# Kernel tuning notes

Measured on AMD Instinct MI355X. Metric: run time of the kernel, lower is better.

The kernel has to match this reference:

```python
import jax, jax.numpy as jnp
import numpy as np

N, E, H, EF, DIM = 50000, 800000, 128, 16, 3
MF = 2 * H + EF + 1 + DIM  # dist_l2 (1) + dist_abs (DIM) = 276


def setup_inputs() -> dict:
    key = jax.random.key(0)
    ks = jax.random.split(key, 16)
    w = lambda k, shape, s=0.05: (jax.random.normal(k, shape, jnp.float32) * s)
    return dict(
        h=jax.random.normal(ks[0], (N, H), jnp.float32),
        coords=jax.random.normal(ks[1], (N, DIM), jnp.float32),
        a=jax.random.normal(ks[2], (E, EF), jnp.float32),
        src=jax.random.randint(ks[3], (E,), 0, N),
        dst=jax.random.randint(ks[4], (E,), 0, N),
        We1=w(ks[5], (MF, H)), be1=jnp.zeros((H,), jnp.float32),
        We2=w(ks[6], (H, H)), be2=jnp.zeros((H,), jnp.float32),
        Wa=w(ks[7], (H, 1)), ba=jnp.zeros((1,), jnp.float32),
        Wn1=w(ks[8], (2 * H, H)), bn1=jnp.zeros((H,), jnp.float32),
        Wn2=w(ks[9], (H, H)), bn2=jnp.zeros((H,), jnp.float32),
        Wc1=w(ks[10], (MF, H)), bc1=jnp.zeros((H,), jnp.float32),
        Wc2=w(ks[11], (H, H)), bc2=jnp.zeros((H,), jnp.float32),
        Wc3=w(ks[12], (H, 1), 0.001),  # xavier gain=0.001, no bias
    )


def reference(h, coords, a, src, dst,
              We1, be1, We2, be2, Wa, ba,
              Wn1, bn1, Wn2, bn2,
              Wc1, bc1, Wc2, bc2, Wc3):
    act = jax.nn.silu
    # gather node data onto edges
    xs, xd = coords[src], coords[dst]          # [E, DIM]
    diffs = xs - xd                            # [E, DIM]
    radials = jnp.linalg.norm(diffs, axis=-1, keepdims=True)  # dist_l2
    D = jnp.concatenate([radials, jnp.abs(diffs)], axis=-1)   # dist_l2, dist_abs
    f = jnp.concatenate([h[src], h[dst], D, a], axis=-1)      # [E, MF]
    # coord_mlp: Lin-act-Lin-act-Lin(no bias)
    cm = act(f @ Wc1 + bc1)
    cm = act(cm @ Wc2 + bc2)
    cm = cm @ Wc3                              # [E, 1]
    msg_x = cm * diffs / (radials + 1.0)       # [E, DIM]
    # edge_mlp + attention gate
    mh = act(f @ We1 + be1)
    mh = act(mh @ We2 + be2)                   # [E, H]
    att = jax.nn.sigmoid(mh @ Wa + ba)         # [E, 1]
    msg_h = att * mh
    # scatter-sum to destination nodes
    x_agg = jax.ops.segment_sum(msg_x, dst, num_segments=N)
    h_agg = jax.ops.segment_sum(msg_h, dst, num_segments=N)
    coords_out = coords + x_agg
    nh = act(jnp.concatenate([h, h_agg], axis=-1) @ Wn1 + bn1) @ Wn2 + bn2
    h_out = h + nh
    return h_out, coords_out
```

## Files before the change

kernel.cpp:

```cpp
#include <hip/hip_runtime.h>
#include <math.h>

#define HH 128
#define HP 64

typedef __attribute__((ext_vector_type(8))) short short8;
typedef __attribute__((ext_vector_type(4))) float float4v;
typedef __attribute__((ext_vector_type(4))) unsigned uint4v;

__device__ __forceinline__ float blo(unsigned w){ return __uint_as_float(w << 16); }
__device__ __forceinline__ float bhi(unsigned w){ return __uint_as_float(w & 0xffff0000u); }
__device__ __forceinline__ unsigned short f2b(float x){
  unsigned u = __float_as_uint(x);
  u += 0x7fffu + ((u >> 16) & 1u);
  return (unsigned short)(u >> 16);
}
__device__ __forceinline__ unsigned pack2(float a, float b){
  return (unsigned)f2b(a) | ((unsigned)f2b(b) << 16);
}
__device__ __forceinline__ float silu_f(float x){ return x / (1.f + __expf(-x)); }

__global__ __launch_bounds__(256, 2) void precompute_mfma_kernel(
    const float* __restrict__ h,
    const float* __restrict__ We1, const float* __restrict__ be1,
    const float* __restrict__ Wc1, const float* __restrict__ bc1,
    unsigned* __restrict__ A1, unsigned* __restrict__ B1,
    unsigned* __restrict__ Ac, unsigned* __restrict__ Bc, int N)
{
  __shared__ unsigned short hs[2][16 * 136];

  const int t = threadIdx.x;
  const int lane = t & 63;
  const int w = t >> 6;
  const int col = lane & 15;
  const int quad = lane >> 4;

  const float* Wsel = (w < 2) ? We1 : Wc1;
  const int kb = (w & 1) * 128;
  unsigned* outp = (w == 0) ? A1 : (w == 1) ? B1 : (w == 2) ? Ac : Bc;
  const float* biasp = (w == 0) ? be1 : (w == 2) ? bc1 : nullptr;

  uint4v wf[8][4];
  #pragma unroll
  for (int nt = 0; nt < 8; ++nt) {
    const int cn = nt * 16 + col;
    #pragma unroll
    for (int ks = 0; ks < 4; ++ks) {
      unsigned u[4];
      #pragma unroll
      for (int i = 0; i < 4; ++i) {
        const int k0 = kb + ks * 32 + quad * 8 + 2 * i;
        u[i] = pack2(Wsel[(size_t)k0 * 128 + cn], Wsel[(size_t)(k0 + 1) * 128 + cn]);
      }
      wf[nt][ks] = (uint4v){u[0], u[1], u[2], u[3]};
    }
  }
  float bias[8];
  #pragma unroll
  for (int nt = 0; nt < 8; ++nt) bias[nt] = biasp ? biasp[nt * 16 + col] : 0.f;

  const int ntiles = (N + 15) >> 4;
  auto stage = [&](int tl, int b) {
    const int n0s = tl * 16;
    for (int idx = t; idx < 16 * 64; idx += 256) {
      const int row = idx >> 6, jp = idx & 63;
      const int n = min(n0s + row, N - 1);
      float2 hv = ((const float2*)h)[(size_t)n * 64 + jp];
      ((unsigned*)&hs[b][row * 136])[jp] = pack2(hv.x, hv.y);
    }
  };

  int tile = blockIdx.x;
  if (tile < ntiles) stage(tile, 0);
  int buf = 0;
  for (; tile < ntiles; tile += gridDim.x, buf ^= 1) {
    __syncthreads();
    if (tile + (int)gridDim.x < ntiles) stage(tile + gridDim.x, buf ^ 1);

    float4v acc[8] = {{0,0,0,0},{0,0,0,0},{0,0,0,0},{0,0,0,0},
                      {0,0,0,0},{0,0,0,0},{0,0,0,0},{0,0,0,0}};
    #pragma unroll
    for (int ks = 0; ks < 4; ++ks) {
      short8 af = __builtin_bit_cast(short8,
          *(const uint4v*)&hs[buf][col * 136 + ks * 32 + quad * 8]);
      #pragma unroll
      for (int nt = 0; nt < 8; ++nt)
        acc[nt] = __builtin_amdgcn_mfma_f32_16x16x32_bf16(
            af, __builtin_bit_cast(short8, wf[nt][ks]), acc[nt], 0, 0, 0);
    }
    const int n0 = tile * 16;
    #pragma unroll
    for (int nt = 0; nt < 8; ++nt) {
      #pragma unroll
      for (int r = 0; r < 4; ++r) {
        float v = acc[nt][r] + bias[nt];
        float o = __shfl_xor(v, 1, 64);
        const int node = n0 + quad * 4 + r;
        if (!(lane & 1) && node < N)
          outp[(size_t)node * HP + ((nt * 16 + col) >> 1)] = pack2(v, o);
      }
    }
  }
}

template<int MODE>
__global__ __launch_bounds__(256, 3) void edge_kernel(
    const unsigned* __restrict__ Apart, const unsigned* __restrict__ Bpart,
    const float* __restrict__ W1,
    const float* __restrict__ W2, const float* __restrict__ b2,
    const float* __restrict__ Wv,
    const float* __restrict__ ba_p,
    const int* __restrict__ src, const int* __restrict__ dst,
    const float* __restrict__ coords, const float* __restrict__ afeat,
    float* __restrict__ out_agg, int E)
{
  __shared__ unsigned short W2Ts[128 * 136];
  __shared__ unsigned short mhl16[32 * 136];
  __shared__ unsigned short tailsA[32 * 40];
  __shared__ float    dif[32 * 4];
  __shared__ int      sl[32], dl[32];
  __shared__ float    p_lds[4][16];

  const int t = threadIdx.x;
  const int lane = t & 63;
  const int w = t >> 6;
  const int mtile = w >> 1;
  const int nhalf = w & 1;
  const int col = lane & 15;
  const int quad = lane >> 4;

  for (int i = t; i < 128 * 128; i += 256) {
    int k = i >> 7, n = i & 127;
    W2Ts[n * 136 + k] = f2b(W2[i]);
  }
  for (int i = t; i < 32 * 20; i += 256) ((unsigned*)tailsA)[i] = 0u;

  uint4v wtf[4];
  #pragma unroll
  for (int nt = 0; nt < 4; ++nt) {
    const int n = nhalf * 64 + nt * 16 + col;
    unsigned u[4];
    #pragma unroll
    for (int i = 0; i < 4; ++i) {
      const int k0 = quad * 8 + 2 * i;
      float a = (k0     < 20) ? W1[(size_t)(256 + k0    ) * 128 + n] : 0.f;
      float b = (k0 + 1 < 20) ? W1[(size_t)(256 + k0 + 1) * 128 + n] : 0.f;
      u[i] = pack2(a, b);
    }
    wtf[nt] = (uint4v){u[0], u[1], u[2], u[3]};
  }
  float b2reg[4], wvreg[4];
  #pragma unroll
  for (int nt = 0; nt < 4; ++nt) {
    const int n = (nhalf * 4 + nt) * 16 + col;
    b2reg[nt] = b2[n];
    wvreg[nt] = Wv[n];
  }
  const float bav = (MODE == 0) ? ba_p[0] : 0.f;
  __syncthreads();

  const int ntiles = (E + 31) >> 5;
  for (int tile = blockIdx.x; tile < ntiles; tile += gridDim.x) {
    const int e0 = tile * 32;
    if (t < 32) {
      int eg = e0 + t;
      int s = 0, d = 0;
      if (eg < E) { s = src[eg]; d = dst[eg]; }
      sl[t] = s; dl[t] = d;
      float dx = coords[s*3+0] - coords[d*3+0];
      float dy = coords[s*3+1] - coords[d*3+1];
      float dz = coords[s*3+2] - coords[d*3+2];
      float rad = sqrtf(dx*dx + dy*dy + dz*dz);
      dif[t*4+0] = dx; dif[t*4+1] = dy; dif[t*4+2] = dz; dif[t*4+3] = rad;
      unsigned* ta = (unsigned*)&tailsA[t * 40];
      ta[0] = pack2(rad, fabsf(dx));
      ta[1] = pack2(fabsf(dy), fabsf(dz));
    }
    #pragma unroll
    for (int i = t; i < 512; i += 256) {
      int e = i >> 4, f = i & 15;
      int eg = e0 + e;
      tailsA[e * 40 + 4 + f] =
          (eg < E) ? f2b(afeat[(size_t)eg * 16 + f]) : (unsigned short)0;
    }
    __syncthreads();

    int er[4], sidx[4], didx[4];
    #pragma unroll
    for (int r = 0; r < 4; ++r) {
      er[r] = mtile * 16 + quad * 4 + r;
      sidx[r] = sl[er[r]]; didx[r] = dl[er[r]];
    }
    const int jbase = nhalf * 32 + (col >> 1);
    unsigned wa32[4][4], wb32[4][4];
    #pragma unroll
    for (int r = 0; r < 4; ++r) {
      const unsigned* ap = Apart + (size_t)sidx[r] * HP + jbase;
      const unsigned* bp = Bpart + (size_t)didx[r] * HP + jbase;
      #pragma unroll
      for (int nt = 0; nt < 4; ++nt) { wa32[r][nt] = ap[nt * 8]; wb32[r][nt] = bp[nt * 8]; }
    }

    float4v acct[4] = {{0,0,0,0},{0,0,0,0},{0,0,0,0},{0,0,0,0}};
    {
      const unsigned short* ap = &tailsA[(mtile * 16 + col) * 40 + quad * 8];
      short8 af = __builtin_bit_cast(short8, *(const uint4v*)ap);
      #pragma unroll
      for (int nt = 0; nt < 4; ++nt)
        acct[nt] = __builtin_amdgcn_mfma_f32_16x16x32_bf16(
            af, __builtin_bit_cast(short8, wtf[nt]), acct[nt], 0, 0, 0);
    }

    const bool hiSel = (col & 1);
    #pragma unroll
    for (int r = 0; r < 4; ++r) {
      #pragma unroll
      for (int nt = 0; nt < 4; ++nt) {
        float va = hiSel ? bhi(wa32[r][nt]) : blo(wa32[r][nt]);
        float vb = hiSel ? bhi(wb32[r][nt]) : blo(wb32[r][nt]);
        float v = va + vb + acct[nt][r];
        mhl16[er[r] * 136 + nhalf * 64 + nt * 16 + col] = f2b(silu_f(v));
      }
    }
    __syncthreads();

    float4v acc[4] = {{0,0,0,0},{0,0,0,0},{0,0,0,0},{0,0,0,0}};
    {
      const unsigned short* abase = &mhl16[(mtile * 16 + col) * 136 + quad * 8];
      #pragma unroll
      for (int ks = 0; ks < 4; ++ks) {
        short8 af = __builtin_bit_cast(short8, *(const uint4v*)(abase + ks * 32));
        #pragma unroll
        for (int nt = 0; nt < 4; ++nt) {
          const unsigned short* bp =
              &W2Ts[((nhalf * 4 + nt) * 16 + col) * 136 + ks * 32 + quad * 8];
          short8 bf = __builtin_bit_cast(short8, *(const uint4v*)bp);
          acc[nt] = __builtin_amdgcn_mfma_f32_16x16x32_bf16(af, bf, acc[nt], 0, 0, 0);
        }
      }
    }

    float p[4] = {0.f, 0.f, 0.f, 0.f};
    #pragma unroll
    for (int nt = 0; nt < 4; ++nt)
      #pragma unroll
      for (int r = 0; r < 4; ++r) {
        float v = silu_f(acc[nt][r] + b2reg[nt]);
        acc[nt][r] = v;
        p[r] += v * wvreg[nt];
      }
    #pragma unroll
    for (int r = 0; r < 4; ++r) {
      #pragma unroll
      for (int off = 1; off < 16; off <<= 1) p[r] += __shfl_xor(p[r], off, 64);
    }
    if (col == 0) {
      #pragma unroll
      for (int r = 0; r < 4; ++r) p_lds[w][quad * 4 + r] = p[r];
    }
    __syncthreads();

    #pragma unroll
    for (int r = 0; r < 4; ++r) {
      const int le = quad * 4 + r;
      const int ei = mtile * 16 + le;
      const int eg = e0 + ei;
      const float pfull = p_lds[w][le] + p_lds[w ^ 1][le];
      if (MODE == 0) {
        if (eg < E) {
          float att = 1.f / (1.f + __expf(-(pfull + bav)));
          int d = dl[ei];
          #pragma unroll
          for (int nt = 0; nt < 4; ++nt) {
            int n = (nhalf * 4 + nt) * 16 + col;
            unsafeAtomicAdd(&out_agg[(size_t)d * HH + n], att * acc[nt][r]);
          }
        }
      } else {
        if (nhalf == 0 && eg < E && col < 3) {
          float rad = dif[ei * 4 + 3];
          float fac = pfull / (rad + 1.f);
          unsafeAtomicAdd(&out_agg[(size_t)dl[ei] * 3 + col], fac * dif[ei * 4 + col]);
        }
      }
    }
    __syncthreads();
  }
}

__global__ __launch_bounds__(256, 4) void node_l1_mfma(
    const float* __restrict__ h, const float* __restrict__ h_agg,
    const float* __restrict__ Wn1, const float* __restrict__ bn1,
    unsigned* __restrict__ g, int N)
{
  __shared__ unsigned short xs[2][16 * 264];

  const int t = threadIdx.x;
  const int lane = t & 63;
  const int w = t >> 6;
  const int col = lane & 15;
  const int quad = lane >> 4;
  const int wbase = w * 32;

  uint4v wf[2][8];
  #pragma unroll
  for (int nt = 0; nt < 2; ++nt) {
    const int cn = wbase + nt * 16 + col;
    #pragma unroll
    for (int ks = 0; ks < 8; ++ks) {
      unsigned u[4];
      #pragma unroll
      for (int i = 0; i < 4; ++i) {
        const int k0 = ks * 32 + quad * 8 + 2 * i;
        u[i] = pack2(Wn1[(size_t)k0 * 128 + cn], Wn1[(size_t)(k0 + 1) * 128 + cn]);
      }
      wf[nt][ks] = (uint4v){u[0], u[1], u[2], u[3]};
    }
  }
  float bias[2] = { bn1[wbase + col], bn1[wbase + 16 + col] };

  const int ntiles = (N + 15) >> 4;
  auto stage = [&](int tl, int b) {
    const int n0s = tl * 16;
    for (int idx = t; idx < 16 * 128; idx += 256) {
      const int row = idx >> 7, jp = idx & 127;
      const int n = min(n0s + row, N - 1);
      float2 v = (jp < 64) ? ((const float2*)h)[(size_t)n * 64 + jp]
                           : ((const float2*)h_agg)[(size_t)n * 64 + (jp - 64)];
      ((unsigned*)&xs[b][row * 264])[jp] = pack2(v.x, v.y);
    }
  };

  int tile = blockIdx.x;
  if (tile < ntiles) stage(tile, 0);
  int buf = 0;
  for (; tile < ntiles; tile += gridDim.x, buf ^= 1) {
    __syncthreads();
    if (tile + (int)gridDim.x < ntiles) stage(tile + gridDim.x, buf ^ 1);

    float4v acc[2] = {{0,0,0,0},{0,0,0,0}};
    #pragma unroll
    for (int ks = 0; ks < 8; ++ks) {
      short8 af = __builtin_bit_cast(short8,
          *(const uint4v*)&xs[buf][col * 264 + ks * 32 + quad * 8]);
      acc[0] = __builtin_amdgcn_mfma_f32_16x16x32_bf16(
          af, __builtin_bit_cast(short8, wf[0][ks]), acc[0], 0, 0, 0);
      acc[1] = __builtin_amdgcn_mfma_f32_16x16x32_bf16(
          af, __builtin_bit_cast(short8, wf[1][ks]), acc[1], 0, 0, 0);
    }
    const int n0 = tile * 16;
    #pragma unroll
    for (int nt = 0; nt < 2; ++nt) {
      #pragma unroll
      for (int r = 0; r < 4; ++r) {
        float v = silu_f(acc[nt][r] + bias[nt]);
        float o = __shfl_xor(v, 1, 64);
        const int node = n0 + quad * 4 + r;
        if (!(lane & 1) && node < N)
          g[(size_t)node * HP + ((wbase + nt * 16 + col) >> 1)] = pack2(v, o);
      }
    }
  }
}

__global__ __launch_bounds__(256, 4) void node_l2_mfma(
    const unsigned* __restrict__ g, const float* __restrict__ h,
    const float* __restrict__ Wn2, const float* __restrict__ bn2,
    float* __restrict__ hout, int N)
{
  const int t = threadIdx.x;
  const int lane = t & 63;
  const int w = t >> 6;
  const int col = lane & 15;
  const int quad = lane >> 4;
  const int wbase = w * 32;

  uint4v wf[2][4];
  #pragma unroll
  for (int nt = 0; nt < 2; ++nt) {
    const int cn = wbase + nt * 16 + col;
    #pragma unroll
    for (int ks = 0; ks < 4; ++ks) {
      unsigned u[4];
      #pragma unroll
      for (int i = 0; i < 4; ++i) {
        const int k0 = ks * 32 + quad * 8 + 2 * i;
        u[i] = pack2(Wn2[(size_t)k0 * 128 + cn], Wn2[(size_t)(k0 + 1) * 128 + cn]);
      }
      wf[nt][ks] = (uint4v){u[0], u[1], u[2], u[3]};
    }
  }
  float bias[2] = { bn2[wbase + col], bn2[wbase + 16 + col] };

  const int ntiles = (N + 15) >> 4;
  for (int tile = blockIdx.x; tile < ntiles; tile += gridDim.x) {
    const int n0 = tile * 16;
    const int na = min(n0 + col, N - 1);

    float4v acc[2] = {{0,0,0,0},{0,0,0,0}};
    #pragma unroll
    for (int ks = 0; ks < 4; ++ks) {
      short8 af = __builtin_bit_cast(short8,
          *(const uint4v*)(g + (size_t)na * HP + ks * 16 + quad * 4));
      acc[0] = __builtin_amdgcn_mfma_f32_16x16x32_bf16(
          af, __builtin_bit_cast(short8, wf[0][ks]), acc[0], 0, 0, 0);
      acc[1] = __builtin_amdgcn_mfma_f32_16x16x32_bf16(
          af, __builtin_bit_cast(short8, wf[1][ks]), acc[1], 0, 0, 0);
    }
    #pragma unroll
    for (int nt = 0; nt < 2; ++nt) {
      const int cn = wbase + nt * 16 + col;
      #pragma unroll
      for (int r = 0; r < 4; ++r) {
        const int node = n0 + quad * 4 + r;
        if (node < N) {
          float v = acc[nt][r] + bias[nt] + h[(size_t)node * HH + cn];
          hout[(size_t)node * HH + cn] = v;
        }
      }
    }
  }
}

__global__ void coords_out_kernel(const float* __restrict__ coords,
                                  const float* __restrict__ x_agg,
                                  float* __restrict__ out, int n3)
{
  int i = blockIdx.x * blockDim.x + threadIdx.x;
  if (i < n3) out[i] = coords[i] + x_agg[i];
}

extern "C" void kernel_launch(void* const* d_in, const int* in_sizes, int n_in,
                              void* d_out, int out_size, void* d_ws, size_t ws_size,
                              hipStream_t stream)
{
  const float* h      = (const float*)d_in[0];
  const float* coords = (const float*)d_in[1];
  const float* afeat  = (const float*)d_in[2];
  const int*   src    = (const int*)d_in[3];
  const int*   dst    = (const int*)d_in[4];
  const float* We1 = (const float*)d_in[5];
  const float* be1 = (const float*)d_in[6];
  const float* We2 = (const float*)d_in[7];
  const float* be2 = (const float*)d_in[8];
  const float* Wa  = (const float*)d_in[9];
  const float* ba  = (const float*)d_in[10];
  const float* Wn1 = (const float*)d_in[11];
  const float* bn1 = (const float*)d_in[12];
  const float* Wn2 = (const float*)d_in[13];
  const float* bn2 = (const float*)d_in[14];
  const float* Wc1 = (const float*)d_in[15];
  const float* bc1 = (const float*)d_in[16];
  const float* Wc2 = (const float*)d_in[17];
  const float* bc2 = (const float*)d_in[18];
  const float* Wc3 = (const float*)d_in[19];

  const int E = in_sizes[3];
  const int N = in_sizes[0] / HH;

  unsigned* A1 = (unsigned*)d_ws;
  unsigned* B1 = A1 + (size_t)N * HP;
  unsigned* Ac = B1 + (size_t)N * HP;
  unsigned* Bc = Ac + (size_t)N * HP;
  float* h_agg = (float*)(Bc + (size_t)N * HP);
  float* x_agg = h_agg + (size_t)N * HH;
  unsigned* gbuf = A1;

  hipMemsetAsync(h_agg, 0, ((size_t)N * HH + (size_t)N * 3) * sizeof(float), stream);

  precompute_mfma_kernel<<<512, 256, 0, stream>>>(h, We1, be1, Wc1, bc1,
                                                  A1, B1, Ac, Bc, N);

  edge_kernel<0><<<768, 256, 0, stream>>>(A1, B1, We1, We2, be2, Wa, ba,
                                          src, dst, coords, afeat, h_agg, E);
  edge_kernel<1><<<768, 256, 0, stream>>>(Ac, Bc, Wc1, Wc2, bc2, Wc3, nullptr,
                                          src, dst, coords, afeat, x_agg, E);

  node_l1_mfma<<<512, 256, 0, stream>>>(h, h_agg, Wn1, bn1, gbuf, N);
  node_l2_mfma<<<1024, 256, 0, stream>>>(gbuf, h, Wn2, bn2, (float*)d_out, N);
  coords_out_kernel<<<(N * 3 + 255) / 256, 256, 0, stream>>>(
      coords, x_agg, (float*)d_out + (size_t)N * HH, N * 3);
}
```

Measured before the change: 836.6 us.

## Software-pipeline edge tile staging and gather loads with triple-buffered LDS

```diff
diff --git a/kernel.cpp b/kernel.cpp
--- a/kernel.cpp
+++ b/kernel.cpp
@@ -97,7 +97,8 @@
         float o = __shfl_xor(v, 1, 64);
         const int node = n0 + quad * 4 + r;
         if (!(lane & 1) && node < N)
-          outp[(size_t)node * HP + ((nt * 16 + col) >> 1)] = pack2(v, o);
+          outp[(size_t)node * HP + (nt >> 2) * 32 + ((col >> 1) << 2) + (nt & 3)]
+              = pack2(v, o);
       }
     }
   }
@@ -116,9 +117,9 @@
 {
   __shared__ unsigned short W2Ts[128 * 136];
   __shared__ unsigned short mhl16[32 * 136];
-  __shared__ unsigned short tailsA[32 * 40];
-  __shared__ float    dif[32 * 4];
-  __shared__ int      sl[32], dl[32];
+  __shared__ unsigned short tailsA[3][32 * 40];
+  __shared__ float    dif[3][32 * 4];
+  __shared__ int      sl[3][32], dl[3][32];
   __shared__ float    p_lds[4][16];
 
   const int t = threadIdx.x;
@@ -133,7 +134,7 @@
     int k = i >> 7, n = i & 127;
     W2Ts[n * 136 + k] = f2b(W2[i]);
   }
-  for (int i = t; i < 32 * 20; i += 256) ((unsigned*)tailsA)[i] = 0u;
+  for (int i = t; i < 3 * 32 * 20; i += 256) ((unsigned*)tailsA)[i] = 0u;
 
   uint4v wtf[4];
   #pragma unroll
@@ -157,53 +158,61 @@
     wvreg[nt] = Wv[n];
   }
   const float bav = (MODE == 0) ? ba_p[0] : 0.f;
-  __syncthreads();
-
-  const int ntiles = (E + 31) >> 5;
-  for (int tile = blockIdx.x; tile < ntiles; tile += gridDim.x) {
-    const int e0 = tile * 32;
+
+  auto stage = [&](int tl, int b) {
+    const int e0s = tl * 32;
     if (t < 32) {
-      int eg = e0 + t;
+      int eg = e0s + t;
       int s = 0, d = 0;
       if (eg < E) { s = src[eg]; d = dst[eg]; }
-      sl[t] = s; dl[t] = d;
+      sl[b][t] = s; dl[b][t] = d;
       float dx = coords[s*3+0] - coords[d*3+0];
       float dy = coords[s*3+1] - coords[d*3+1];
       float dz = coords[s*3+2] - coords[d*3+2];
       float rad = sqrtf(dx*dx + dy*dy + dz*dz);
-      dif[t*4+0] = dx; dif[t*4+1] = dy; dif[t*4+2] = dz; dif[t*4+3] = rad;
-      unsigned* ta = (unsigned*)&tailsA[t * 40];
+      dif[b][t*4+0] = dx; dif[b][t*4+1] = dy;
+      dif[b][t*4+2] = dz; dif[b][t*4+3] = rad;
+      unsigned* ta = (unsigned*)&tailsA[b][t * 40];
       ta[0] = pack2(rad, fabsf(dx));
       ta[1] = pack2(fabsf(dy), fabsf(dz));
     }
-    #pragma unroll
-    for (int i = t; i < 512; i += 256) {
-      int e = i >> 4, f = i & 15;
-      int eg = e0 + e;
-      tailsA[e * 40 + 4 + f] =
-          (eg < E) ? f2b(afeat[(size_t)eg * 16 + f]) : (unsigned short)0;
-    }
-    __syncthreads();
-
-    int er[4], sidx[4], didx[4];
+    if (t < 128) {
+      int e = t >> 2, q4 = t & 3;
+      int eg = e0s + e;
+      float4 v = make_float4(0.f, 0.f, 0.f, 0.f);
+      if (eg < E) v = ((const float4*)afeat)[(size_t)eg * 4 + q4];
+      unsigned* d4 = (unsigned*)&tailsA[b][e * 40 + 4 + q4 * 4];
+      d4[0] = pack2(v.x, v.y);
+      d4[1] = pack2(v.z, v.w);
+    }
+  };
+
+  const int gs = gridDim.x;
+  const int ntiles = (E + 31) >> 5;
+  const int T0 = blockIdx.x;
+  if (T0 < ntiles)      stage(T0, 0);
+  if (T0 + gs < ntiles) stage(T0 + gs, 1);
+  __syncthreads();
+
+  uint4v wa4[4], wb4[4];
+  const int jb4 = nhalf * 32 + ((col >> 1) << 2);
+  auto issueG = [&](int b) {
     #pragma unroll
     for (int r = 0; r < 4; ++r) {
-      er[r] = mtile * 16 + quad * 4 + r;
-      sidx[r] = sl[er[r]]; didx[r] = dl[er[r]];
-    }
-    const int jbase = nhalf * 32 + (col >> 1);
-    unsigned wa32[4][4], wb32[4][4];
-    #pragma unroll
-    for (int r = 0; r < 4; ++r) {
-      const unsigned* ap = Apart + (size_t)sidx[r] * HP + jbase;
-      const unsigned* bp = Bpart + (size_t)didx[r] * HP + jbase;
-      #pragma unroll
-      for (int nt = 0; nt < 4; ++nt) { wa32[r][nt] = ap[nt * 8]; wb32[r][nt] = bp[nt * 8]; }
-    }
+      const int e = mtile * 16 + quad * 4 + r;
+      wa4[r] = *(const uint4v*)(Apart + (size_t)sl[b][e] * HP + jb4);
+      wb4[r] = *(const uint4v*)(Bpart + (size_t)dl[b][e] * HP + jb4);
+    }
+  };
+  if (T0 < ntiles) issueG(0);
+
+  int buf = 0;
+  for (int tile = T0; tile < ntiles; tile += gs, buf = (buf == 2) ? 0 : buf + 1) {
+    const int e0 = tile * 32;
 
     float4v acct[4] = {{0,0,0,0},{0,0,0,0},{0,0,0,0},{0,0,0,0}};
     {
-      const unsigned short* ap = &tailsA[(mtile * 16 + col) * 40 + quad * 8];
+      const unsigned short* ap = &tailsA[buf][(mtile * 16 + col) * 40 + quad * 8];
       short8 af = __builtin_bit_cast(short8, *(const uint4v*)ap);
       #pragma unroll
       for (int nt = 0; nt < 4; ++nt)
@@ -214,15 +223,19 @@
     const bool hiSel = (col & 1);
     #pragma unroll
     for (int r = 0; r < 4; ++r) {
+      const int er_ = mtile * 16 + quad * 4 + r;
       #pragma unroll
       for (int nt = 0; nt < 4; ++nt) {
-        float va = hiSel ? bhi(wa32[r][nt]) : blo(wa32[r][nt]);
-        float vb = hiSel ? bhi(wb32[r][nt]) : blo(wb32[r][nt]);
+        unsigned ua = wa4[r][nt], ub = wb4[r][nt];
+        float va = hiSel ? bhi(ua) : blo(ua);
+        float vb = hiSel ? bhi(ub) : blo(ub);
         float v = va + vb + acct[nt][r];
-        mhl16[er[r] * 136 + nhalf * 64 + nt * 16 + col] = f2b(silu_f(v));
+        mhl16[er_ * 136 + nhalf * 64 + nt * 16 + col] = f2b(silu_f(v));
       }
     }
     __syncthreads();
+
+    if (tile + 2 * gs < ntiles) stage(tile + 2 * gs, (buf == 0) ? 2 : buf - 1);
 
     float4v acc[4] = {{0,0,0,0},{0,0,0,0},{0,0,0,0},{0,0,0,0}};
     {
@@ -260,6 +273,8 @@
     }
     __syncthreads();
 
+    if (tile + gs < ntiles) issueG((buf == 2) ? 0 : buf + 1);
+
     #pragma unroll
     for (int r = 0; r < 4; ++r) {
       const int le = quad * 4 + r;
@@ -269,7 +284,7 @@
       if (MODE == 0) {
         if (eg < E) {
           float att = 1.f / (1.f + __expf(-(pfull + bav)));
-          int d = dl[ei];
+          int d = dl[buf][ei];
           #pragma unroll
           for (int nt = 0; nt < 4; ++nt) {
             int n = (nhalf * 4 + nt) * 16 + col;
@@ -278,13 +293,13 @@
         }
       } else {
         if (nhalf == 0 && eg < E && col < 3) {
-          float rad = dif[ei * 4 + 3];
+          float rad = dif[buf][ei * 4 + 3];
           float fac = pfull / (rad + 1.f);
-          unsafeAtomicAdd(&out_agg[(size_t)dl[ei] * 3 + col], fac * dif[ei * 4 + col]);
+          unsafeAtomicAdd(&out_agg[(size_t)dl[buf][ei] * 3 + col],
+                          fac * dif[buf][ei * 4 + col]);
         }
       }
     }
-    __syncthreads();
   }
 }
 
```

New measurement: 785.8 us. 6.1% less time.
